# Performance work log

Hardware: AMD Instinct MI355X
Metric: run time of the kernel (lower is better)

## Reference

```python
import jax, jax.numpy as jnp
import numpy as np


def _dwconv3x3(x, w, b):
    # depthwise 3x3, stride 1, padding 1 (groups == channels)
    y = jax.lax.conv_general_dilated(
        x, w, window_strides=(1, 1), padding=((1, 1), (1, 1)),
        dimension_numbers=('NCHW', 'OIHW', 'NCHW'),
        feature_group_count=x.shape[1])
    return y + b[None, :, None, None]


def _maxpool(x, f):
    # adaptive_max_pool2d to (h//f, w//f) with h,w divisible by f == stride-f max pool
    return jax.lax.reduce_window(x, -jnp.inf, jax.lax.max,
                                 (1, 1, f, f), (1, 1, f, f), 'VALID')


def _up_nearest(x, f):
    return jnp.repeat(jnp.repeat(x, f, axis=2), f, axis=3)


def setup_inputs() -> dict:
    key = jax.random.key(0)
    ks = jax.random.split(key, 10)
    B, C, H, W = 4, 32, 128, 128
    x = jax.random.normal(ks[0], (B, C, H, W), dtype=jnp.float32)
    mk = lambda k, shape, s: jax.random.normal(k, shape, dtype=jnp.float32) * s
    return {
        'x': x,
        'w0': mk(ks[1], (C, 1, 3, 3), 0.3), 'b0': mk(ks[2], (C,), 0.05),
        'w1': mk(ks[3], (C, 1, 3, 3), 0.3), 'b1': mk(ks[4], (C,), 0.05),
        'w2': mk(ks[5], (C, 1, 3, 3), 0.3), 'b2': mk(ks[6], (C,), 0.05),
        'wa': mk(ks[7], (C, C, 1, 1), 0.2), 'ba': mk(ks[8], (C,), 0.05),
    }


def reference(x, w0, b0, w1, b1, w2, b2, wa, ba):
    b, c, h, w = x.shape
    # multi-scale depthwise feature refinement
    s0 = _dwconv3x3(x, w0, b0)                               # level 0: full res
    s1 = _up_nearest(_dwconv3x3(_maxpool(x, 2), w1, b1), 2)  # level 1: /2
    s2 = _up_nearest(_dwconv3x3(_maxpool(x, 4), w2, b2), 4)  # level 2: /4
    # Channel_mixing8: q=s0, k=s1, v=s2; per-pixel CxC outer product
    to_nc = lambda t: t.transpose(0, 2, 3, 1).reshape(-1, c)  # (N, C), N=b*h*w
    q, k, v = to_nc(s0), to_nc(s1), to_nc(s2)
    kv = v[:, :, None] * k[:, None, :]        # (N, C, C) = v_embed @ k_embed^T
    attn = jax.nn.softmax(kv, axis=1)         # softmax over dim=1 (v axis)
    qkv = jnp.einsum('nij,nj->ni', attn, q)   # matvec with q
    out = qkv.reshape(b, h, w, c).transpose(0, 3, 1, 2)
    # aggr: 1x1 conv; drop_path=0 -> identity
    out = jnp.einsum('bchw,oc->bohw', out, wa[:, :, 0, 0]) + ba[None, :, None, None]
    return jax.nn.gelu(out, approximate=False) * x
```

## Files before the change

kernel.cpp:

```cpp
#include <hip/hip_runtime.h>
#include <hip/hip_fp16.h>
#include <math.h>


typedef _Float16 half2_t __attribute__((ext_vector_type(2)));

__device__ __forceinline__ half2_t bch2(unsigned int u) {
  return __builtin_bit_cast(half2_t, u);
}
__device__ __forceinline__ float fdot2(unsigned int a, unsigned int b, float c) {
  return __builtin_amdgcn_fdot2(bch2(a), bch2(b), c, false);
}

__device__ __forceinline__ int QS(int p) { return p * 64 + (((p >> 2) & 7) << 2); }

__global__ __launch_bounds__(256) void fused_safm(
    const float* __restrict__ x,
    const float* __restrict__ w0, const float* __restrict__ b0,
    const float* __restrict__ w1, const float* __restrict__ b1,
    const float* __restrict__ w2, const float* __restrict__ b2,
    const float* __restrict__ wa, const float* __restrict__ ba,
    float* __restrict__ out) {
  int bid = blockIdx.x;
  int tw = bid & 7, th = (bid >> 3) & 63, b = bid >> 9;
  int t = threadIdx.x;
  int h4 = th >> 1;

  __shared__ __align__(16) unsigned int regA[4128];
  __shared__ __align__(16) unsigned int qrdsh[544];
  __shared__ __align__(16) float s0s[1056];
  __shared__ __align__(16) float vsh[288];
  __shared__ __align__(16) float qkvs[2048];
  float* p1s = (float*)regA;

  {
    const float* xb = x + ((size_t)(b * 32) << 14);
#pragma unroll
    for (int k = 0; k < 3; ++k) {
      int idx = t + k * 256;
      if (idx < 576) {
        int c = idx / 18, rem = idx % 18;
        int r = rem / 3, s = rem % 3;
        int pr = 2 * h4 - 2 + r;
        int pc0 = 8 * tw - 2 + 4 * s;
        float m0 = 0.f, m1 = 0.f, m2 = 0.f, m3 = 0.f;
        if ((unsigned)pr < 64u) {
          const float* xp = xb + ((size_t)c << 14) + (2 * pr) * 128;
          if (pc0 >= 0 && pc0 + 3 < 64) {
            const float* q = xp + 2 * pc0;
            float4 a0 = *(const float4*)q;
            float4 a1 = *(const float4*)(q + 4);
            float4 c0 = *(const float4*)(q + 128);
            float4 c1 = *(const float4*)(q + 132);
            m0 = fmaxf(fmaxf(a0.x, a0.y), fmaxf(c0.x, c0.y));
            m1 = fmaxf(fmaxf(a0.z, a0.w), fmaxf(c0.z, c0.w));
            m2 = fmaxf(fmaxf(a1.x, a1.y), fmaxf(c1.x, c1.y));
            m3 = fmaxf(fmaxf(a1.z, a1.w), fmaxf(c1.z, c1.w));
          } else {
            float mm[4] = {0.f, 0.f, 0.f, 0.f};
#pragma unroll
            for (int m_ = 0; m_ < 4; ++m_) {
              int pc = pc0 + m_;
              if ((unsigned)pc < 64u) {
                const float* q = xp + 2 * pc;
                float2 r0 = *(const float2*)q;
                float2 r1 = *(const float2*)(q + 128);
                mm[m_] = fmaxf(fmaxf(r0.x, r0.y), fmaxf(r1.x, r1.y));
              }
            }
            m0 = mm[0]; m1 = mm[1]; m2 = mm[2]; m3 = mm[3];
          }
        }
        *(float4*)(p1s + c * 76 + r * 12 + 4 * s) = make_float4(m0, m1, m2, m3);
      }
    }
  }
  {
    int c = t >> 3, gg = t & 7;
    int hh = gg >> 2, wb = (gg & 3) * 4;
    const float* xp = x + ((size_t)(b * 32 + c) << 14);
    const float* wc = w0 + c * 9;
    float wv[9];
#pragma unroll
    for (int q = 0; q < 9; ++q) wv[q] = wc[q];
    float bz = b0[c];
    float a0 = bz, a1 = bz, a2 = bz, a3 = bz;
    int cbase = 16 * tw + wb;
#pragma unroll
    for (int dr = -1; dr <= 1; ++dr) {
      int row = 2 * th + hh + dr;
      if ((unsigned)row >= 128u) continue;
      const float* rp = xp + row * 128 + cbase;
      float cm1 = (cbase > 0)       ? rp[-1] : 0.f;
      float4 c03 = *(const float4*)rp;
      float c4  = (cbase + 4 < 128) ? rp[4]  : 0.f;
      float wA = wv[(dr + 1) * 3], wB = wv[(dr + 1) * 3 + 1], wC = wv[(dr + 1) * 3 + 2];
      a0 = fmaf(wA, cm1,   fmaf(wB, c03.x, fmaf(wC, c03.y, a0)));
      a1 = fmaf(wA, c03.x, fmaf(wB, c03.y, fmaf(wC, c03.z, a1)));
      a2 = fmaf(wA, c03.y, fmaf(wB, c03.z, fmaf(wC, c03.w, a2)));
      a3 = fmaf(wA, c03.z, fmaf(wB, c03.w, fmaf(wC, c4,    a3)));
    }
    int pb = hh * 16 + wb;
    s0s[(pb)     * 33 + c] = a0;
    s0s[(pb + 1) * 33 + c] = a1;
    s0s[(pb + 2) * 33 + c] = a2;
    s0s[(pb + 3) * 33 + c] = a3;
  }
  __syncthreads();

  int ebT = t >> 5, jT = t & 31;
  float kreg;
  {
    const float* wc = w1 + jT * 9;
    const float* Pk = p1s + jT * 76 + ((th & 1) + 1) * 12 + ebT + 1;
    float acc = b1[jT];
    acc = fmaf(wc[0], Pk[0],  fmaf(wc[1], Pk[1],  fmaf(wc[2], Pk[2],  acc)));
    acc = fmaf(wc[3], Pk[12], fmaf(wc[4], Pk[13], fmaf(wc[5], Pk[14], acc)));
    acc = fmaf(wc[6], Pk[24], fmaf(wc[7], Pk[25], fmaf(wc[8], Pk[26], acc)));
    kreg = acc;
  }
  {
    const float* wc = w2 + jT * 9;
    const float* P = p1s + jT * 76 + 2 * (ebT >> 1);
    float acc = b2[jT];
#pragma unroll
    for (int hq = 0; hq < 3; ++hq) {
      const float* Pr = P + 2 * hq * 12;
#pragma unroll
      for (int wq = 0; wq < 3; ++wq) {
        float2 u0 = *(const float2*)(Pr + 2 * wq);
        float2 u1 = *(const float2*)(Pr + 2 * wq + 12);
        float p2v = fmaxf(fmaxf(u0.x, u0.y), fmaxf(u1.x, u1.y));
        acc = fmaf(wc[hq * 3 + wq], p2v, acc);
      }
    }
    vsh[ebT * 36 + jT] = acc;
  }
  __syncthreads();

  {
    const float* vb = vsh + ebT * 36;
    const float4* v4 = (const float4*)vb;
    float4 q0 = v4[0];
    float vmax = fmaxf(fmaxf(q0.x, q0.y), fmaxf(q0.z, q0.w));
    float vmin = fminf(fminf(q0.x, q0.y), fminf(q0.z, q0.w));
#pragma unroll
    for (int iq = 1; iq < 8; ++iq) {
      float4 q_ = v4[iq];
      vmax = fmaxf(vmax, fmaxf(fmaxf(q_.x, q_.y), fmaxf(q_.z, q_.w)));
      vmin = fminf(vmin, fminf(fminf(q_.x, q_.y), fminf(q_.z, q_.w)));
    }
    const float L2E = 1.4426950408889634f;
    float m  = (kreg >= 0.f) ? kreg * vmax : kreg * vmin;
    float kl = kreg * L2E;
    float nm = -m * L2E;
    float d0 = 0.f, d1 = 0.f;
    __half* Eh = (__half*)regA;
    int colbase = ebT * 1032 + jT;
#pragma unroll
    for (int ip = 0; ip < 16; ++ip) {
      float2 vp = *(const float2*)(vb + 2 * ip);
      float e0 = __builtin_amdgcn_exp2f(fmaf(vp.x, kl, nm));
      float e1 = __builtin_amdgcn_exp2f(fmaf(vp.y, kl, nm));
      d0 += e0; d1 += e1;
      Eh[colbase + (2 * ip) * 32]     = __float2half(e0);
      Eh[colbase + (2 * ip + 1) * 32] = __float2half(e1);
    }
    float rd = __fdividef(1.f, d0 + d1);
    __half* Qh = (__half*)qrdsh;
    int qbase = ebT * 136 + jT;
#pragma unroll
    for (int px = 0; px < 4; ++px) {
      int hh = px >> 1, wwb = px & 1;
      int p = hh * 16 + ebT * 2 + wwb;
      float qv = s0s[p * 33 + jT] * rd;
      Qh[qbase + px * 32] = __float2half(qv);
    }
  }
  __syncthreads();

  {
    int p = t & 31, ic = t >> 5;
    int eb = (p & 15) >> 1;
    int px = 2 * (p >> 4) + (p & 1);
    const uint4* Eq = (const uint4*)(regA + eb * 516);
    const uint4* Uq = (const uint4*)(qrdsh + eb * 68 + px * 16);
    uint4 u0 = Uq[0], u1 = Uq[1], u2 = Uq[2], u3 = Uq[3];
    float a0, a1, a2, a3;
#define SAFM_ROW(di, dst)                                              \
    {                                                                  \
      const uint4* Er = Eq + (4 * ic + di) * 4;                        \
      uint4 w0_ = Er[0], w1_ = Er[1], w2_ = Er[2], w3_ = Er[3];        \
      float s_ = 0.f;                                                  \
      s_ = fdot2(w0_.x, u0.x, s_); s_ = fdot2(w0_.y, u0.y, s_);        \
      s_ = fdot2(w0_.z, u0.z, s_); s_ = fdot2(w0_.w, u0.w, s_);        \
      s_ = fdot2(w1_.x, u1.x, s_); s_ = fdot2(w1_.y, u1.y, s_);        \
      s_ = fdot2(w1_.z, u1.z, s_); s_ = fdot2(w1_.w, u1.w, s_);        \
      s_ = fdot2(w2_.x, u2.x, s_); s_ = fdot2(w2_.y, u2.y, s_);        \
      s_ = fdot2(w2_.z, u2.z, s_); s_ = fdot2(w2_.w, u2.w, s_);        \
      s_ = fdot2(w3_.x, u3.x, s_); s_ = fdot2(w3_.y, u3.y, s_);        \
      s_ = fdot2(w3_.z, u3.z, s_); s_ = fdot2(w3_.w, u3.w, s_);        \
      dst = s_;                                                        \
    }
    SAFM_ROW(0, a0) SAFM_ROW(1, a1) SAFM_ROW(2, a2) SAFM_ROW(3, a3)
#undef SAFM_ROW
    *(float4*)(qkvs + QS(p) + 4 * ic) = make_float4(a0, a1, a2, a3);
  }
  __syncthreads();

  {
    int o = t >> 3, g = t & 7;
    int hh = g >> 2, wb = (g & 3) * 4;
    const float* wo = wa + o * 32;
    const float* qA = qkvs + QS(hh * 16 + wb);
    const float* qB = qkvs + QS(hh * 16 + wb + 1);
    const float* qC = qkvs + QS(hh * 16 + wb + 2);
    const float* qD = qkvs + QS(hh * 16 + wb + 3);
    float bz = ba[o];
    float y0 = bz, y1 = bz, y2 = bz, y3 = bz;
#pragma unroll
    for (int m = 0; m < 8; ++m) {
      float4 fA = *(const float4*)(qA + 4 * m);
      float4 fB = *(const float4*)(qB + 4 * m);
      float4 fC = *(const float4*)(qC + 4 * m);
      float4 fD = *(const float4*)(qD + 4 * m);
      float wv0 = wo[4 * m], wv1 = wo[4 * m + 1], wv2 = wo[4 * m + 2], wv3 = wo[4 * m + 3];
      y0 = fmaf(wv0, fA.x, fmaf(wv1, fA.y, fmaf(wv2, fA.z, fmaf(wv3, fA.w, y0))));
      y1 = fmaf(wv0, fB.x, fmaf(wv1, fB.y, fmaf(wv2, fB.z, fmaf(wv3, fB.w, y1))));
      y2 = fmaf(wv0, fC.x, fmaf(wv1, fC.y, fmaf(wv2, fC.z, fmaf(wv3, fC.w, y2))));
      y3 = fmaf(wv0, fD.x, fmaf(wv1, fD.y, fmaf(wv2, fD.z, fmaf(wv3, fD.w, y3))));
    }
    const float RS2 = 0.70710678118654752f;
    float g0 = 0.5f * y0 * (1.f + erff(y0 * RS2));
    float g1 = 0.5f * y1 * (1.f + erff(y1 * RS2));
    float g2 = 0.5f * y2 * (1.f + erff(y2 * RS2));
    float g3 = 0.5f * y3 * (1.f + erff(y3 * RS2));
    size_t ob = (((size_t)(b * 32 + o) * 128) + (2 * th + hh)) * 128 + 16 * tw + wb;
    float4 xv = *(const float4*)(x + ob);
    float4 r;
    r.x = g0 * xv.x; r.y = g1 * xv.y; r.z = g2 * xv.z; r.w = g3 * xv.w;
    *(float4*)(out + ob) = r;
  }
}

extern "C" void kernel_launch(void* const* d_in, const int* in_sizes, int n_in,
                              void* d_out, int out_size, void* d_ws, size_t ws_size,
                              hipStream_t stream) {
  const float* x  = (const float*)d_in[0];
  const float* w0 = (const float*)d_in[1];
  const float* b0 = (const float*)d_in[2];
  const float* w1 = (const float*)d_in[3];
  const float* b1 = (const float*)d_in[4];
  const float* w2 = (const float*)d_in[5];
  const float* b2 = (const float*)d_in[6];
  const float* wa = (const float*)d_in[7];
  const float* ba = (const float*)d_in[8];
  float* out = (float*)d_out;

  fused_safm<<<2048, 256, 0, stream>>>(x, w0, b0, w1, b1, w2, b2, wa, ba, out);
}
```

Before: 105.5 us.

## Recompute softmax exponentials in matvec stage instead of storing fp16 table

The softmax stage no longer writes a 32x32 fp16 exponential table to shared memory per 4-pixel group. It stores only the per-column scale and offset (kl, nm) and the normalized q values in fp32. The matvec stage then recomputes each exponential on the fly with exp2 and accumulates with fp32 FMAs instead of fdot2. This cuts shared-memory footprint and traffic and drops fp16 precision loss, at the cost of computing each exponential twice, since the denominators still need them.

```diff
diff --git a/kernel.cpp b/kernel.cpp
--- a/kernel.cpp
+++ b/kernel.cpp
@@ -1,16 +1,6 @@
 #include <hip/hip_runtime.h>
-#include <hip/hip_fp16.h>
 #include <math.h>
 
-
-typedef _Float16 half2_t __attribute__((ext_vector_type(2)));
-
-__device__ __forceinline__ half2_t bch2(unsigned int u) {
-  return __builtin_bit_cast(half2_t, u);
-}
-__device__ __forceinline__ float fdot2(unsigned int a, unsigned int b, float c) {
-  return __builtin_amdgcn_fdot2(bch2(a), bch2(b), c, false);
-}
 
 __device__ __forceinline__ int QS(int p) { return p * 64 + (((p >> 2) & 7) << 2); }
 
@@ -26,12 +16,13 @@
   int t = threadIdx.x;
   int h4 = th >> 1;
 
-  __shared__ __align__(16) unsigned int regA[4128];
-  __shared__ __align__(16) unsigned int qrdsh[544];
+  __shared__ __align__(16) float regAB[2432];
+  __shared__ __align__(16) float klns[512];
+  __shared__ __align__(16) float qds[1024];
   __shared__ __align__(16) float s0s[1056];
   __shared__ __align__(16) float vsh[288];
-  __shared__ __align__(16) float qkvs[2048];
-  float* p1s = (float*)regA;
+  float* p1s  = regAB;
+  float* qkvs = regAB;
 
   {
     const float* xb = x + ((size_t)(b * 32) << 14);
@@ -155,56 +146,56 @@
     float kl = kreg * L2E;
     float nm = -m * L2E;
     float d0 = 0.f, d1 = 0.f;
-    __half* Eh = (__half*)regA;
-    int colbase = ebT * 1032 + jT;
 #pragma unroll
     for (int ip = 0; ip < 16; ++ip) {
       float2 vp = *(const float2*)(vb + 2 * ip);
-      float e0 = __builtin_amdgcn_exp2f(fmaf(vp.x, kl, nm));
-      float e1 = __builtin_amdgcn_exp2f(fmaf(vp.y, kl, nm));
-      d0 += e0; d1 += e1;
-      Eh[colbase + (2 * ip) * 32]     = __float2half(e0);
-      Eh[colbase + (2 * ip + 1) * 32] = __float2half(e1);
+      d0 += __builtin_amdgcn_exp2f(fmaf(vp.x, kl, nm));
+      d1 += __builtin_amdgcn_exp2f(fmaf(vp.y, kl, nm));
     }
     float rd = __fdividef(1.f, d0 + d1);
-    __half* Qh = (__half*)qrdsh;
-    int qbase = ebT * 136 + jT;
-#pragma unroll
-    for (int px = 0; px < 4; ++px) {
-      int hh = px >> 1, wwb = px & 1;
-      int p = hh * 16 + ebT * 2 + wwb;
-      float qv = s0s[p * 33 + jT] * rd;
-      Qh[qbase + px * 32] = __float2half(qv);
-    }
-  }
-  __syncthreads();
-
-  {
-    int p = t & 31, ic = t >> 5;
-    int eb = (p & 15) >> 1;
-    int px = 2 * (p >> 4) + (p & 1);
-    const uint4* Eq = (const uint4*)(regA + eb * 516);
-    const uint4* Uq = (const uint4*)(qrdsh + eb * 68 + px * 16);
-    uint4 u0 = Uq[0], u1 = Uq[1], u2 = Uq[2], u3 = Uq[3];
-    float a0, a1, a2, a3;
-#define SAFM_ROW(di, dst)                                              \
-    {                                                                  \
-      const uint4* Er = Eq + (4 * ic + di) * 4;                        \
-      uint4 w0_ = Er[0], w1_ = Er[1], w2_ = Er[2], w3_ = Er[3];        \
-      float s_ = 0.f;                                                  \
-      s_ = fdot2(w0_.x, u0.x, s_); s_ = fdot2(w0_.y, u0.y, s_);        \
-      s_ = fdot2(w0_.z, u0.z, s_); s_ = fdot2(w0_.w, u0.w, s_);        \
-      s_ = fdot2(w1_.x, u1.x, s_); s_ = fdot2(w1_.y, u1.y, s_);        \
-      s_ = fdot2(w1_.z, u1.z, s_); s_ = fdot2(w1_.w, u1.w, s_);        \
-      s_ = fdot2(w2_.x, u2.x, s_); s_ = fdot2(w2_.y, u2.y, s_);        \
-      s_ = fdot2(w2_.z, u2.z, s_); s_ = fdot2(w2_.w, u2.w, s_);        \
-      s_ = fdot2(w3_.x, u3.x, s_); s_ = fdot2(w3_.y, u3.y, s_);        \
-      s_ = fdot2(w3_.z, u3.z, s_); s_ = fdot2(w3_.w, u3.w, s_);        \
-      dst = s_;                                                        \
-    }
-    SAFM_ROW(0, a0) SAFM_ROW(1, a1) SAFM_ROW(2, a2) SAFM_ROW(3, a3)
-#undef SAFM_ROW
-    *(float4*)(qkvs + QS(p) + 4 * ic) = make_float4(a0, a1, a2, a3);
+    *(float2*)(klns + (ebT * 32 + jT) * 2) = make_float2(kl, nm);
+    float4 qv;
+    qv.x = s0s[(ebT * 2)      * 33 + jT] * rd;
+    qv.y = s0s[(ebT * 2 + 1)  * 33 + jT] * rd;
+    qv.z = s0s[(ebT * 2 + 16) * 33 + jT] * rd;
+    qv.w = s0s[(ebT * 2 + 17) * 33 + jT] * rd;
+    *(float4*)(qds + (ebT * 32 + jT) * 4) = qv;
+  }
+  __syncthreads();
+
+  {
+    int i = t & 31, eb = t >> 5;
+    float vi = vsh[eb * 36 + i];
+    const float* klp = klns + eb * 64;
+    const float* qdp = qds + eb * 128;
+    float a0 = 0.f, a1 = 0.f, a2 = 0.f, a3 = 0.f;
+#pragma unroll
+    for (int jw = 0; jw < 8; ++jw) {
+      float4 k01 = *(const float4*)(klp + jw * 8);
+      float4 k23 = *(const float4*)(klp + jw * 8 + 4);
+      float4 qd0 = *(const float4*)(qdp + jw * 16);
+      float4 qd1 = *(const float4*)(qdp + jw * 16 + 4);
+      float4 qd2 = *(const float4*)(qdp + jw * 16 + 8);
+      float4 qd3 = *(const float4*)(qdp + jw * 16 + 12);
+      float e;
+      e = __builtin_amdgcn_exp2f(fmaf(vi, k01.x, k01.y));
+      a0 = fmaf(e, qd0.x, a0); a1 = fmaf(e, qd0.y, a1);
+      a2 = fmaf(e, qd0.z, a2); a3 = fmaf(e, qd0.w, a3);
+      e = __builtin_amdgcn_exp2f(fmaf(vi, k01.z, k01.w));
+      a0 = fmaf(e, qd1.x, a0); a1 = fmaf(e, qd1.y, a1);
+      a2 = fmaf(e, qd1.z, a2); a3 = fmaf(e, qd1.w, a3);
+      e = __builtin_amdgcn_exp2f(fmaf(vi, k23.x, k23.y));
+      a0 = fmaf(e, qd2.x, a0); a1 = fmaf(e, qd2.y, a1);
+      a2 = fmaf(e, qd2.z, a2); a3 = fmaf(e, qd2.w, a3);
+      e = __builtin_amdgcn_exp2f(fmaf(vi, k23.z, k23.w));
+      a0 = fmaf(e, qd3.x, a0); a1 = fmaf(e, qd3.y, a1);
+      a2 = fmaf(e, qd3.z, a2); a3 = fmaf(e, qd3.w, a3);
+    }
+    int p0 = eb * 2;
+    qkvs[QS(p0)      + i] = a0;
+    qkvs[QS(p0 + 1)  + i] = a1;
+    qkvs[QS(p0 + 16) + i] = a2;
+    qkvs[QS(p0 + 17) + i] = a3;
   }
   __syncthreads();
 
```

Result: faster. 102.9 us (-2.5%).
